# Kernel tuning notes

Measured on AMD Instinct MI355X. Metric: run time of the kernel, lower is better.

Reference implementation:

```python
import jax, jax.numpy as jnp
import numpy as np
import math

B, S, D = 16, 512, 1024
H, L = 16, 4
DH = D // H
EPS = 1e-5


def _layernorm(x, w, b):
    mu = jnp.mean(x, axis=-1, keepdims=True)
    var = jnp.mean(jnp.square(x - mu), axis=-1, keepdims=True)
    return (x - mu) / jnp.sqrt(var + EPS) * w + b


def _pos_encoding(s, d):
    pos = jnp.arange(s, dtype=jnp.float32)[:, None]                      # [s,1]
    div = jnp.exp(jnp.arange(0, d, 2, dtype=jnp.float32) * (-math.log(10000.0) / d))
    ang = pos * div[None, :]                                             # [s,d/2]
    return jnp.stack([jnp.sin(ang), jnp.cos(ang)], axis=-1).reshape(s, d)  # interleave sin/cos


def _attention_layer(x, Wq, bq, Wv, bv, Wo, bo, gamma, ln_w, ln_b, mask):
    bs, s, d = x.shape
    # q_linear == k_linear (kq_same=True)
    q = (x @ Wq.T + bq).reshape(bs, s, H, DH).transpose(0, 2, 1, 3)      # [b,h,s,dh]
    k = q
    v = (x @ Wv.T + bv).reshape(bs, s, H, DH).transpose(0, 2, 1, 3)

    scores = jnp.einsum('bhqd,bhkd->bhqk', q, k) / math.sqrt(DH)         # [b,h,s,s]

    # distance-decay modulation (dist_scores is detached in the original)
    p = jax.nn.softmax(jnp.where(mask, scores, -1e32), axis=-1)
    distcum = jnp.cumsum(p, axis=-1)
    disttot = jnp.sum(p, axis=-1, keepdims=True)
    idx = jnp.arange(s, dtype=jnp.float32)
    pos_eff = jnp.abs(idx[None, :] - idx[:, None])[None, None, :, :]     # |i-j|
    dist = jnp.sqrt(jnp.maximum((disttot - distcum) * pos_eff, 0.0))
    dist = jax.lax.stop_gradient(dist)

    g = -jnp.abs(gamma)[None, :, None, None]                             # [1,h,1,1]
    total_effect = jnp.clip(jnp.exp(dist * g), 1e-5, 1e5)
    scores = scores * total_effect

    scores = jnp.where(mask, scores, -1e32)
    attn = jax.nn.softmax(scores, axis=-1)
    attn = jnp.where(mask, attn, 0.0)

    # maxout=True (peek_cur=False): clamp(1/max, max=5)
    scale = jnp.minimum(1.0 / jnp.max(attn, axis=-1, keepdims=True), 5.0)
    attn = attn * scale

    out = jnp.einsum('bhqk,bhkd->bhqd', attn, v)                         # [b,h,s,dh]
    out = out.transpose(0, 2, 1, 3).reshape(bs, s, d)
    out = out @ Wo.T + bo

    # eval mode: dropout = identity; residual + layernorm
    return _layernorm(x + out, ln_w, ln_b), attn


def reference(x, lens, Wq, bq, Wv, bv, Wo, bo, gammas, ln_w, ln_b, fln_w, fln_b):
    del lens  # only used in training-mode random masking
    s = x.shape[1]
    q = x + _pos_encoding(s, D)[None, :, :]
    mask = jnp.tril(jnp.ones((s, s), dtype=bool), -1)[None, None, :, :]  # peek_cur=False
    scores = None
    for l in range(L):
        q, scores = _attention_layer(q, Wq[l], bq[l], Wv[l], bv[l], Wo[l], bo[l],
                                     gammas[l], ln_w[l], ln_b[l], mask)
    return _layernorm(q, fln_w, fln_b), scores


def setup_inputs() -> dict:
    key = jax.random.key(0)
    ks = jax.random.split(key, 8)
    wscale = 1.0 / math.sqrt(D)
    return {
        'x': jax.random.normal(ks[0], (B, S, D), dtype=jnp.float32),
        'lens': jax.random.randint(ks[1], (B,), 1, S),
        'Wq': jax.random.normal(ks[2], (L, D, D), dtype=jnp.float32) * wscale,
        'bq': jnp.zeros((L, D), dtype=jnp.float32),
        'Wv': jax.random.normal(ks[3], (L, D, D), dtype=jnp.float32) * wscale,
        'bv': jnp.zeros((L, D), dtype=jnp.float32),
        'Wo': jax.random.normal(ks[4], (L, D, D), dtype=jnp.float32) * wscale,
        'bo': jnp.zeros((L, D), dtype=jnp.float32),
        'gammas': jax.random.uniform(ks[5], (L, H), dtype=jnp.float32, minval=-1.7, maxval=1.7),
        'ln_w': jnp.ones((L, D), dtype=jnp.float32),
        'ln_b': jnp.zeros((L, D), dtype=jnp.float32),
        'fln_w': jnp.ones((D,), dtype=jnp.float32),
        'fln_b': jnp.zeros((D,), dtype=jnp.float32),
    }
```

## Files before the change

kernel.cpp:

```cpp
#include <hip/hip_runtime.h>
#include <hip/hip_bf16.h>

#define BB 16
#define SS 512
#define DD 1024
#define HH 16
#define LL 4
#define DHH 64
#define GK 1024

typedef __attribute__((ext_vector_type(8))) short short8;
typedef __attribute__((ext_vector_type(4))) float f32x4;

__device__ __forceinline__ unsigned short f2bf(float f) {
  union { float f; unsigned int u; } v; v.f = f;
  unsigned int r = v.u + 0x7FFFu + ((v.u >> 16) & 1u);
  return (unsigned short)(r >> 16);
}
__device__ __forceinline__ float bf2f(unsigned short u) {
  union { unsigned int i; float f; } v; v.i = ((unsigned)u) << 16; return v.f;
}

__device__ __forceinline__ float wave_max(float v) {
#pragma unroll
  for (int off = 32; off > 0; off >>= 1) v = fmaxf(v, __shfl_xor(v, off));
  return v;
}
__device__ __forceinline__ float wave_sum(float v) {
#pragma unroll
  for (int off = 32; off > 0; off >>= 1) v += __shfl_xor(v, off);
  return v;
}
__device__ __forceinline__ float half_max(float v) {
#pragma unroll
  for (int off = 16; off > 0; off >>= 1) v = fmaxf(v, __shfl_xor(v, off));
  return v;
}
__device__ __forceinline__ float half_sum(float v) {
#pragma unroll
  for (int off = 16; off > 0; off >>= 1) v += __shfl_xor(v, off);
  return v;
}

__device__ __forceinline__ void gl16(const void* g, void* l) {
  __builtin_amdgcn_global_load_lds(
      (const __attribute__((address_space(1))) unsigned int*)(uintptr_t)g,
      (__attribute__((address_space(3))) unsigned int*)(unsigned int)(uintptr_t)l,
      16, 0, 0);
}

__global__ __launch_bounds__(256) void k_w2bf_all(
    const float* __restrict__ wq, const float* __restrict__ wv,
    const float* __restrict__ wo, unsigned short* __restrict__ oqv,
    unsigned short* __restrict__ oo) {
  size_t i4 = ((size_t)blockIdx.x * 256 + threadIdx.x) * 4;
  const size_t QV = (size_t)2 * LL * DD * DD;
  const float* src;
  unsigned short* dst;
  if (i4 < QV) {
    size_t l = i4 >> 21;
    size_t r = i4 & ((1u << 21) - 1);
    src = (r < (1u << 20)) ? wq + (l << 20) + r
                           : wv + (l << 20) + (r - (1u << 20));
    dst = oqv + i4;
  } else {
    size_t j = i4 - QV;
    src = wo + j;
    dst = oo + j;
  }
  float4 v = *(const float4*)src;
  uint2 pk;
  pk.x = (unsigned)f2bf(v.x) | ((unsigned)f2bf(v.y) << 16);
  pk.y = (unsigned)f2bf(v.z) | ((unsigned)f2bf(v.w) << 16);
  *(uint2*)dst = pk;
}

__global__ __launch_bounds__(256) void k_add_pe(const float* __restrict__ x,
                                                unsigned short* __restrict__ outb) {
  size_t i4 = ((size_t)blockIdx.x * 256 + threadIdx.x) * 4;
  int d0 = (int)(i4 & (DD - 1));
  int s = (int)((i4 >> 10) & (SS - 1));
  float4 xv = *(const float4*)(x + i4);
  int ip0 = d0 >> 1;
  float f0 = __expf((float)ip0 * -0.017988946039016f);
  float f1 = __expf((float)(ip0 + 1) * -0.017988946039016f);
  float s0v, c0v, s1v, c1v;
  __sincosf((float)s * f0, &s0v, &c0v);
  __sincosf((float)s * f1, &s1v, &c1v);
  float o0 = xv.x + s0v, o1 = xv.y + c0v, o2 = xv.z + s1v, o3 = xv.w + c1v;
  uint2 pk;
  pk.x = (unsigned)f2bf(o0) | ((unsigned)f2bf(o1) << 16);
  pk.y = (unsigned)f2bf(o2) | ((unsigned)f2bf(o3) << 16);
  *(uint2*)(outb + i4) = pk;
}

template <int MODE>
__global__ __launch_bounds__(256) void k_gemm(
    const unsigned short* __restrict__ A, const unsigned short* __restrict__ W,
    const float* __restrict__ bias, const float* __restrict__ bias2,
    void* __restrict__ out, void* __restrict__ out2) {
  __shared__ unsigned short As[2][128 * 32];
  __shared__ unsigned short Bs[2][128 * 32];
  const int tid = threadIdx.x;
  const int lane = tid & 63;
  const int w = tid >> 6;
  const int wr = w >> 1, wc = w & 1;
  const int fr = lane & 15, fq = lane >> 4;

  int bid = blockIdx.x;
  const int cpx = gridDim.x >> 3;
  bid = (bid & 7) * cpx + (bid >> 3);
  const int bm = (bid & 63) * 128;
  const int bn = (bid >> 6) * 128;

  f32x4 acc[4][4] = {};

  const unsigned short* ga = A + (size_t)(bm + w * 16 + (lane >> 2)) * GK + (lane & 3) * 8;
  const unsigned short* gb = W + (size_t)(bn + w * 16 + (lane >> 2)) * GK + (lane & 3) * 8;

  auto STAGE = [&](int buf, int k0) {
    unsigned short* la = As[buf] + w * 512;
    unsigned short* lb = Bs[buf] + w * 512;
    gl16(ga + k0, la);
    gl16(ga + 64 * GK + k0, la + 2048);
    gl16(gb + k0, lb);
    gl16(gb + 64 * GK + k0, lb + 2048);
  };

  STAGE(0, 0);
  __syncthreads();
  int cur = 0;
  for (int k0 = 0; k0 < GK; k0 += 32) {
    if (k0 + 32 < GK) STAGE(cur ^ 1, k0 + 32);
    short8 af[4], bf[4];
#pragma unroll
    for (int m = 0; m < 4; ++m)
      af[m] = *(const short8*)(As[cur] + (wr * 64 + m * 16 + fr) * 32 + fq * 8);
#pragma unroll
    for (int n = 0; n < 4; ++n)
      bf[n] = *(const short8*)(Bs[cur] + (wc * 64 + n * 16 + fr) * 32 + fq * 8);
#pragma unroll
    for (int m = 0; m < 4; ++m)
#pragma unroll
      for (int n = 0; n < 4; ++n)
        acc[m][n] = __builtin_amdgcn_mfma_f32_16x16x32_bf16(af[m], bf[n], acc[m][n], 0, 0, 0);
    __syncthreads();
    cur ^= 1;
  }

#pragma unroll
  for (int m = 0; m < 4; ++m) {
    const int row0 = bm + wr * 64 + m * 16 + fq * 4;
#pragma unroll
    for (int n = 0; n < 4; ++n) {
      const int col = bn + wc * 64 + n * 16 + fr;
      if constexpr (MODE == 0) {
        const float bsv = bias[col];
        unsigned short* o = (unsigned short*)out;
#pragma unroll
        for (int r = 0; r < 4; ++r)
          o[(size_t)(row0 + r) * DD + col] = f2bf(acc[m][n][r] + bsv);
      } else {
        if (col < DD) {
          const float bsv = bias[col];
          unsigned short* o = (unsigned short*)out;
#pragma unroll
          for (int r = 0; r < 4; ++r)
            o[(size_t)(row0 + r) * DD + col] = f2bf(acc[m][n][r] + bsv);
        } else {
          const int c2 = col - DD;
          const float bsv = bias2[c2];
          unsigned short* o = (unsigned short*)out2;
          const int bi = row0 >> 9, si = row0 & (SS - 1);
          uint2 pk;
          pk.x = (unsigned)f2bf(acc[m][n][0] + bsv) | ((unsigned)f2bf(acc[m][n][1] + bsv) << 16);
          pk.y = (unsigned)f2bf(acc[m][n][2] + bsv) | ((unsigned)f2bf(acc[m][n][3] + bsv) << 16);
          *(uint2*)(o + ((size_t)bi * DD + c2) * SS + si) = pk;
        }
      }
    }
  }
}

__global__ __launch_bounds__(512) void k_attn(
    const unsigned short* __restrict__ Q, const unsigned short* __restrict__ Vt,
    const float* __restrict__ gam, unsigned short* __restrict__ AO,
    float* __restrict__ scores_out) {
  __shared__ float sc_s[32][516];
  __shared__ unsigned short KV[64][72];

  const int tid = threadIdx.x;
  const int lane = tid & 63;
  const int w = tid >> 6;
  const int wr = w & 1;
  const int wc = w >> 1;
  const int fr = lane & 15, fq = lane >> 4;

  const int itile = 15 - (blockIdx.x >> 8);
  const int bh = blockIdx.x & 255;
  const int b = bh >> 4;
  const int h = bh & 15;
  const int i0 = itile * 32;
  const int njt = (itile + 2) >> 1;
  const int jcap = njt * 64;

  const unsigned short* Qb = Q + (size_t)b * SS * DD + h * DHH;
  const unsigned short* Vtb = Vt + ((size_t)b * DD + h * DHH) * SS;
  const float gneg = -fabsf(gam[h]);

  const int srow = tid >> 3;
  const int sdb = (tid & 7) * 8;

  const unsigned short* qrow = Qb + (size_t)(i0 + wr * 16 + fr) * DD;
  short8 a0 = *(const short8*)(qrow + fq * 8);
  short8 a1 = *(const short8*)(qrow + 32 + fq * 8);

  short8 kreg = *(const short8*)(Qb + (size_t)srow * DD + sdb);
  for (int jt = 0; jt < njt; ++jt) {
    *(short8*)&KV[srow][sdb] = kreg;
    const unsigned short* nsrc = (jt + 1 < njt)
        ? Qb + (size_t)((jt + 1) * 64 + srow) * DD + sdb
        : Vtb + (size_t)srow * SS + sdb;
    kreg = *(const short8*)nsrc;
    __syncthreads();

    short8 b0 = *(const short8*)&KV[wc * 16 + fr][fq * 8];
    short8 b1 = *(const short8*)&KV[wc * 16 + fr][32 + fq * 8];
    f32x4 s0 = {};
    __builtin_amdgcn_s_setprio(1);
    s0 = __builtin_amdgcn_mfma_f32_16x16x32_bf16(a0, b0, s0, 0, 0, 0);
    s0 = __builtin_amdgcn_mfma_f32_16x16x32_bf16(a1, b1, s0, 0, 0, 0);
    __builtin_amdgcn_s_setprio(0);

    const int j = jt * 64 + wc * 16 + fr;
#pragma unroll
    for (int r = 0; r < 4; ++r) {
      const int row = wr * 16 + fq * 4 + r;
      sc_s[row][j] = (j < i0 + row) ? s0[r] * 0.125f : -1e30f;
    }
    __syncthreads();
  }
  *(short8*)&KV[srow][sdb] = kreg;

  if (itile >= 8) {
    const int jb = lane << 3;
#pragma unroll 2
    for (int q = 0; q < 4; ++q) {
      const int r_i = w * 4 + q;
      const int gi = i0 + r_i;
      const float* rowp = &sc_s[r_i][0];
      float4 v0 = *(const float4*)(rowp + jb);
      float4 v1 = *(const float4*)(rowp + jb + 4);
      float sc[8] = {v0.x, v0.y, v0.z, v0.w, v1.x, v1.y, v1.z, v1.w};
#pragma unroll
      for (int c = 0; c < 8; ++c)
        if (jb + c >= jcap) sc[c] = -1e30f;

      float p[8];
      float lsum = 0.0f;
#pragma unroll
      for (int c = 0; c < 8; ++c) {
        p[c] = __expf(sc[c]);
        lsum += p[c];
      }

      float xs = lsum;
#pragma unroll
      for (int off = 1; off < 64; off <<= 1) {
        float y = __shfl_up(xs, off);
        if (lane >= off) xs += y;
      }
      const float tot = __shfl(xs, 63);
      const float inv = 1.0f / tot;
      float run = xs - lsum;

      float s2[8];
#pragma unroll
      for (int c = 0; c < 8; ++c) {
        run += p[c];
        float cum = run * inv;
        float dist = sqrtf(fmaxf((1.0f - cum) * (float)(gi - (jb + c)), 0.0f));
        float te = __expf(gneg * dist);
        te = fminf(fmaxf(te, 1e-5f), 1e5f);
        s2[c] = sc[c] * te;
      }

      float m2 = s2[0];
#pragma unroll
      for (int c = 1; c < 8; ++c) m2 = fmaxf(m2, s2[c]);
      m2 = wave_max(m2);
      float e[8];
      float lsum2 = 0.0f;
#pragma unroll
      for (int c = 0; c < 8; ++c) {
        e[c] = __expf(s2[c] - m2);
        lsum2 += e[c];
      }
      float tot2 = wave_sum(lsum2);
      float mult = fminf(tot2, 5.0f) / tot2;

      float av[8];
#pragma unroll
      for (int c = 0; c < 8; ++c) av[c] = (gi == 0) ? 0.0f : e[c] * mult;

      if (scores_out) {
        float* so = scores_out + ((size_t)(b * HH + h) * SS + gi) * SS + jb;
        *(float4*)(so) = make_float4(av[0], av[1], av[2], av[3]);
        *(float4*)(so + 4) = make_float4(av[4], av[5], av[6], av[7]);
      }

      short8 pk;
#pragma unroll
      for (int c = 0; c < 8; ++c) pk[c] = (short)f2bf(av[c]);
      *(short8*)((unsigned short*)&sc_s[r_i][0] + jb) = pk;
    }
  } else {
    const int half = lane >> 5;
    const int ll = lane & 31;
    const int jb = ll << 3;
    for (int q = 0; q < 2; ++q) {
      const int r_i = w * 4 + q * 2 + half;
      const int gi = i0 + r_i;
      const float* rowp = &sc_s[r_i][0];
      float4 v0 = *(const float4*)(rowp + jb);
      float4 v1 = *(const float4*)(rowp + jb + 4);
      float sc[8] = {v0.x, v0.y, v0.z, v0.w, v1.x, v1.y, v1.z, v1.w};
#pragma unroll
      for (int c = 0; c < 8; ++c)
        if (jb + c >= jcap) sc[c] = -1e30f;

      float p[8];
      float lsum = 0.0f;
#pragma unroll
      for (int c = 0; c < 8; ++c) {
        p[c] = __expf(sc[c]);
        lsum += p[c];
      }

      float xs = lsum;
#pragma unroll
      for (int off = 1; off < 32; off <<= 1) {
        float y = __shfl_up(xs, off, 32);
        if (ll >= off) xs += y;
      }
      const float tot = __shfl(xs, 31, 32);
      const float inv = 1.0f / tot;
      float run = xs - lsum;

      float s2[8];
#pragma unroll
      for (int c = 0; c < 8; ++c) {
        run += p[c];
        float cum = run * inv;
        float dist = sqrtf(fmaxf((1.0f - cum) * (float)(gi - (jb + c)), 0.0f));
        float te = __expf(gneg * dist);
        te = fminf(fmaxf(te, 1e-5f), 1e5f);
        s2[c] = sc[c] * te;
      }

      float m2 = s2[0];
#pragma unroll
      for (int c = 1; c < 8; ++c) m2 = fmaxf(m2, s2[c]);
      m2 = half_max(m2);
      float e[8];
      float lsum2 = 0.0f;
#pragma unroll
      for (int c = 0; c < 8; ++c) {
        e[c] = __expf(s2[c] - m2);
        lsum2 += e[c];
      }
      const float tot2 = half_sum(lsum2);
      const float mult = fminf(tot2, 5.0f) / tot2;

      float av[8];
#pragma unroll
      for (int c = 0; c < 8; ++c) av[c] = (gi == 0) ? 0.0f : e[c] * mult;

      if (scores_out) {
        float* so = scores_out + ((size_t)(b * HH + h) * SS + gi) * SS + jb;
        *(float4*)(so) = make_float4(av[0], av[1], av[2], av[3]);
        *(float4*)(so + 4) = make_float4(av[4], av[5], av[6], av[7]);
        *(float4*)(so + 256) = make_float4(0.f, 0.f, 0.f, 0.f);
        *(float4*)(so + 260) = make_float4(0.f, 0.f, 0.f, 0.f);
      }

      short8 pk;
#pragma unroll
      for (int c = 0; c < 8; ++c) pk[c] = (short)f2bf(av[c]);
      *(short8*)((unsigned short*)&sc_s[r_i][0] + jb) = pk;
    }
  }
  __syncthreads();

  short8 vreg;
  if (njt > 1) vreg = *(const short8*)(Vtb + (size_t)srow * SS + 64 + sdb);
  f32x4 o0 = {};
  for (int jt = 0; jt < njt; ++jt) {
    const unsigned short* arow = (const unsigned short*)&sc_s[wr * 16 + fr][0];
    short8 pa0 = *(const short8*)(arow + jt * 64 + fq * 8);
    short8 pa1 = *(const short8*)(arow + jt * 64 + 32 + fq * 8);
    short8 c0 = *(const short8*)&KV[wc * 16 + fr][fq * 8];
    short8 c1 = *(const short8*)&KV[wc * 16 + fr][32 + fq * 8];
    __builtin_amdgcn_s_setprio(1);
    o0 = __builtin_amdgcn_mfma_f32_16x16x32_bf16(pa0, c0, o0, 0, 0, 0);
    o0 = __builtin_amdgcn_mfma_f32_16x16x32_bf16(pa1, c1, o0, 0, 0, 0);
    __builtin_amdgcn_s_setprio(0);
    __syncthreads();
    if (jt + 1 < njt) {
      *(short8*)&KV[srow][sdb] = vreg;
      if (jt + 2 < njt) vreg = *(const short8*)(Vtb + (size_t)srow * SS + (jt + 2) * 64 + sdb);
      __syncthreads();
    }
  }

  {
    const int d = h * DHH + wc * 16 + fr;
#pragma unroll
    for (int r = 0; r < 4; ++r) {
      const int row = i0 + wr * 16 + fq * 4 + r;
      AO[((size_t)b * SS + row) * DD + d] = f2bf(o0[r]);
    }
  }
}

__global__ __launch_bounds__(256) void k_res_ln(
    const unsigned short* __restrict__ x, const unsigned short* __restrict__ r,
    const float* __restrict__ w, const float* __restrict__ b,
    unsigned short* __restrict__ outb, float* __restrict__ outf) {
  __shared__ float red[4];
  const int row = blockIdx.x;
  const int tid = threadIdx.x;
  const int lane = tid & 63, wv = tid >> 6;
  uint2 xa = ((const uint2*)(x + (size_t)row * DD))[tid];
  float y0 = bf2f((unsigned short)xa.x);
  float y1 = bf2f((unsigned short)(xa.x >> 16));
  float y2 = bf2f((unsigned short)xa.y);
  float y3 = bf2f((unsigned short)(xa.y >> 16));
  if (r) {
    uint2 ra = ((const uint2*)(r + (size_t)row * DD))[tid];
    y0 += bf2f((unsigned short)ra.x);
    y1 += bf2f((unsigned short)(ra.x >> 16));
    y2 += bf2f((unsigned short)ra.y);
    y3 += bf2f((unsigned short)(ra.y >> 16));
  }
  float s = y0 + y1 + y2 + y3;
  s = wave_sum(s);
  if (lane == 0) red[wv] = s;
  __syncthreads();
  float mean = (red[0] + red[1] + red[2] + red[3]) * (1.0f / DD);
  __syncthreads();
  float d0 = y0 - mean, d1 = y1 - mean, d2 = y2 - mean, d3 = y3 - mean;
  float s2 = d0 * d0 + d1 * d1 + d2 * d2 + d3 * d3;
  s2 = wave_sum(s2);
  if (lane == 0) red[wv] = s2;
  __syncthreads();
  float var = (red[0] + red[1] + red[2] + red[3]) * (1.0f / DD);
  float rstd = rsqrtf(var + 1e-5f);
  float4 ww = ((const float4*)w)[tid];
  float4 bb = ((const float4*)b)[tid];
  float o0 = d0 * rstd * ww.x + bb.x;
  float o1 = d1 * rstd * ww.y + bb.y;
  float o2 = d2 * rstd * ww.z + bb.z;
  float o3 = d3 * rstd * ww.w + bb.w;
  if (outf) {
    ((float4*)(outf + (size_t)row * DD))[tid] = make_float4(o0, o1, o2, o3);
  } else {
    uint2 pk;
    pk.x = (unsigned)f2bf(o0) | ((unsigned)f2bf(o1) << 16);
    pk.y = (unsigned)f2bf(o2) | ((unsigned)f2bf(o3) << 16);
    ((uint2*)(outb + (size_t)row * DD))[tid] = pk;
  }
}

extern "C" void kernel_launch(void* const* d_in, const int* in_sizes, int n_in,
                              void* d_out, int out_size, void* d_ws, size_t ws_size,
                              hipStream_t stream) {
  (void)in_sizes; (void)n_in; (void)out_size; (void)ws_size;
  const float* x = (const float*)d_in[0];
  const float* Wq = (const float*)d_in[2];
  const float* bq = (const float*)d_in[3];
  const float* Wv = (const float*)d_in[4];
  const float* bv = (const float*)d_in[5];
  const float* Wo = (const float*)d_in[6];
  const float* bo = (const float*)d_in[7];
  const float* gam = (const float*)d_in[8];
  const float* lnw = (const float*)d_in[9];
  const float* lnb = (const float*)d_in[10];
  const float* flnw = (const float*)d_in[11];
  const float* flnb = (const float*)d_in[12];

  float* out0 = (float*)d_out;
  float* scores = out0 + (size_t)BB * SS * DD;
  const size_t BUF = (size_t)BB * SS * DD;
  const size_t WSZ = (size_t)LL * DD * DD;
  const size_t BHSS = (size_t)BB * HH * SS * SS;

  unsigned short* us = (unsigned short*)d_ws;
  unsigned short* Abf0 = us;
  unsigned short* Abf1 = us + BUF;
  unsigned short* Qbf = us + 2 * BUF;
  unsigned short* VtB = us + 3 * BUF;
  unsigned short* AObf = us + 4 * BUF;
  unsigned short* Pb = us + 5 * BUF;
  unsigned short* Wob = us + 6 * BUF;
  unsigned short* Wqvb = (unsigned short*)scores + (2 * BHSS - 2 * WSZ);

  const int M = BB * SS;

  k_w2bf_all<<<dim3(3 * WSZ / 1024), 256, 0, stream>>>(Wq, Wv, Wo, Wqvb, Wob);
  k_add_pe<<<dim3(BUF / 1024), 256, 0, stream>>>(x, Abf0);

  unsigned short* Acur = Abf0;
  unsigned short* Anx = Abf1;
  for (int l = 0; l < LL; ++l) {
    float* sc_dst = (l == LL - 1) ? scores : nullptr;
    k_gemm<3><<<dim3(1024), 256, 0, stream>>>(Acur, Wqvb + (size_t)l * 2048 * DD,
                                              bq + l * DD, bv + l * DD, Qbf, VtB);
    k_attn<<<dim3(BB * HH * 16), 512, 0, stream>>>(Qbf, VtB, gam + l * HH, AObf, sc_dst);
    k_gemm<0><<<dim3(512), 256, 0, stream>>>(AObf, Wob + (size_t)l * DD * DD,
                                             bo + l * DD, nullptr, Pb, nullptr);
    k_res_ln<<<dim3(M), 256, 0, stream>>>(Acur, Pb, lnw + l * DD, lnb + l * DD, Anx, nullptr);
    unsigned short* t = Acur; Acur = Anx; Anx = t;
  }
  k_res_ln<<<dim3(M), 256, 0, stream>>>(Acur, nullptr, flnw, flnb, nullptr, out0);
}
```

Baseline: 820.8 us.

## Double attention query tile to 64 rows and store scores in fp16 LDS

The attention kernel now handles 64 query rows per block instead of 32. Each wave computes two 16-column MFMA tiles, and the grid is halved. Score staging in shared memory moves from fp32 to fp16 so the larger tile fits in about the same LDS footprint. Each K/V tile loaded into LDS is now reused by twice as many query rows, which cuts global reloads and the number of blocks. In exchange, causal tiles get coarser (more wasted work on the diagonal) and intermediate scores lose precision to fp16 before the softmax.

After: 786.7 us. 1.04x faster.

```diff
diff --git a/kernel.cpp b/kernel.cpp
--- a/kernel.cpp
+++ b/kernel.cpp
@@ -11,6 +11,7 @@
 
 typedef __attribute__((ext_vector_type(8))) short short8;
 typedef __attribute__((ext_vector_type(4))) float f32x4;
+typedef __attribute__((ext_vector_type(8))) _Float16 half8;
 
 __device__ __forceinline__ unsigned short f2bf(float f) {
   union { float f; unsigned int u; } v; v.f = f;
@@ -186,22 +187,22 @@
     const unsigned short* __restrict__ Q, const unsigned short* __restrict__ Vt,
     const float* __restrict__ gam, unsigned short* __restrict__ AO,
     float* __restrict__ scores_out) {
-  __shared__ float sc_s[32][516];
+  __shared__ _Float16 sc_s[64][520];
   __shared__ unsigned short KV[64][72];
 
   const int tid = threadIdx.x;
   const int lane = tid & 63;
   const int w = tid >> 6;
-  const int wr = w & 1;
-  const int wc = w >> 1;
+  const int wr = w & 3;
+  const int wc = w >> 2;
   const int fr = lane & 15, fq = lane >> 4;
 
-  const int itile = 15 - (blockIdx.x >> 8);
+  const int itile = 7 - (blockIdx.x >> 8);
   const int bh = blockIdx.x & 255;
   const int b = bh >> 4;
   const int h = bh & 15;
-  const int i0 = itile * 32;
-  const int njt = (itile + 2) >> 1;
+  const int i0 = itile * 64;
+  const int njt = itile + 1;
   const int jcap = njt * 64;
 
   const unsigned short* Qb = Q + (size_t)b * SS * DD + h * DHH;
@@ -224,34 +225,42 @@
     kreg = *(const short8*)nsrc;
     __syncthreads();
 
-    short8 b0 = *(const short8*)&KV[wc * 16 + fr][fq * 8];
-    short8 b1 = *(const short8*)&KV[wc * 16 + fr][32 + fq * 8];
-    f32x4 s0 = {};
+    short8 b00 = *(const short8*)&KV[wc * 32 + fr][fq * 8];
+    short8 b01 = *(const short8*)&KV[wc * 32 + fr][32 + fq * 8];
+    short8 b10 = *(const short8*)&KV[wc * 32 + 16 + fr][fq * 8];
+    short8 b11 = *(const short8*)&KV[wc * 32 + 16 + fr][32 + fq * 8];
+    f32x4 s0 = {}, s1 = {};
     __builtin_amdgcn_s_setprio(1);
-    s0 = __builtin_amdgcn_mfma_f32_16x16x32_bf16(a0, b0, s0, 0, 0, 0);
-    s0 = __builtin_amdgcn_mfma_f32_16x16x32_bf16(a1, b1, s0, 0, 0, 0);
+    s0 = __builtin_amdgcn_mfma_f32_16x16x32_bf16(a0, b00, s0, 0, 0, 0);
+    s0 = __builtin_amdgcn_mfma_f32_16x16x32_bf16(a1, b01, s0, 0, 0, 0);
+    s1 = __builtin_amdgcn_mfma_f32_16x16x32_bf16(a0, b10, s1, 0, 0, 0);
+    s1 = __builtin_amdgcn_mfma_f32_16x16x32_bf16(a1, b11, s1, 0, 0, 0);
     __builtin_amdgcn_s_setprio(0);
 
-    const int j = jt * 64 + wc * 16 + fr;
-#pragma unroll
-    for (int r = 0; r < 4; ++r) {
-      const int row = wr * 16 + fq * 4 + r;
-      sc_s[row][j] = (j < i0 + row) ? s0[r] * 0.125f : -1e30f;
+#pragma unroll
+    for (int n = 0; n < 2; ++n) {
+      const int j = jt * 64 + wc * 32 + n * 16 + fr;
+#pragma unroll
+      for (int r = 0; r < 4; ++r) {
+        const int row = wr * 16 + fq * 4 + r;
+        const float val = (n ? s1[r] : s0[r]) * 0.125f;
+        sc_s[row][j] = (j < i0 + row) ? (_Float16)val : (_Float16)(-65504.0f);
+      }
     }
     __syncthreads();
   }
   *(short8*)&KV[srow][sdb] = kreg;
 
-  if (itile >= 8) {
+  if (itile >= 4) {
     const int jb = lane << 3;
 #pragma unroll 2
-    for (int q = 0; q < 4; ++q) {
-      const int r_i = w * 4 + q;
+    for (int q = 0; q < 8; ++q) {
+      const int r_i = w * 8 + q;
       const int gi = i0 + r_i;
-      const float* rowp = &sc_s[r_i][0];
-      float4 v0 = *(const float4*)(rowp + jb);
-      float4 v1 = *(const float4*)(rowp + jb + 4);
-      float sc[8] = {v0.x, v0.y, v0.z, v0.w, v1.x, v1.y, v1.z, v1.w};
+      half8 hv = *(const half8*)(&sc_s[r_i][0] + jb);
+      float sc[8];
+#pragma unroll
+      for (int c = 0; c < 8; ++c) sc[c] = (float)hv[c];
 #pragma unroll
       for (int c = 0; c < 8; ++c)
         if (jb + c >= jcap) sc[c] = -1e30f;
@@ -318,13 +327,13 @@
     const int half = lane >> 5;
     const int ll = lane & 31;
     const int jb = ll << 3;
-    for (int q = 0; q < 2; ++q) {
-      const int r_i = w * 4 + q * 2 + half;
+    for (int q = 0; q < 4; ++q) {
+      const int r_i = w * 8 + q * 2 + half;
       const int gi = i0 + r_i;
-      const float* rowp = &sc_s[r_i][0];
-      float4 v0 = *(const float4*)(rowp + jb);
-      float4 v1 = *(const float4*)(rowp + jb + 4);
-      float sc[8] = {v0.x, v0.y, v0.z, v0.w, v1.x, v1.y, v1.z, v1.w};
+      half8 hv = *(const half8*)(&sc_s[r_i][0] + jb);
+      float sc[8];
+#pragma unroll
+      for (int c = 0; c < 8; ++c) sc[c] = (float)hv[c];
 #pragma unroll
       for (int c = 0; c < 8; ++c)
         if (jb + c >= jcap) sc[c] = -1e30f;
@@ -394,16 +403,20 @@
 
   short8 vreg;
   if (njt > 1) vreg = *(const short8*)(Vtb + (size_t)srow * SS + 64 + sdb);
-  f32x4 o0 = {};
+  f32x4 o0 = {}, o1 = {};
   for (int jt = 0; jt < njt; ++jt) {
     const unsigned short* arow = (const unsigned short*)&sc_s[wr * 16 + fr][0];
     short8 pa0 = *(const short8*)(arow + jt * 64 + fq * 8);
     short8 pa1 = *(const short8*)(arow + jt * 64 + 32 + fq * 8);
-    short8 c0 = *(const short8*)&KV[wc * 16 + fr][fq * 8];
-    short8 c1 = *(const short8*)&KV[wc * 16 + fr][32 + fq * 8];
+    short8 c00 = *(const short8*)&KV[wc * 32 + fr][fq * 8];
+    short8 c01 = *(const short8*)&KV[wc * 32 + fr][32 + fq * 8];
+    short8 c10 = *(const short8*)&KV[wc * 32 + 16 + fr][fq * 8];
+    short8 c11 = *(const short8*)&KV[wc * 32 + 16 + fr][32 + fq * 8];
     __builtin_amdgcn_s_setprio(1);
-    o0 = __builtin_amdgcn_mfma_f32_16x16x32_bf16(pa0, c0, o0, 0, 0, 0);
-    o0 = __builtin_amdgcn_mfma_f32_16x16x32_bf16(pa1, c1, o0, 0, 0, 0);
+    o0 = __builtin_amdgcn_mfma_f32_16x16x32_bf16(pa0, c00, o0, 0, 0, 0);
+    o0 = __builtin_amdgcn_mfma_f32_16x16x32_bf16(pa1, c01, o0, 0, 0, 0);
+    o1 = __builtin_amdgcn_mfma_f32_16x16x32_bf16(pa0, c10, o1, 0, 0, 0);
+    o1 = __builtin_amdgcn_mfma_f32_16x16x32_bf16(pa1, c11, o1, 0, 0, 0);
     __builtin_amdgcn_s_setprio(0);
     __syncthreads();
     if (jt + 1 < njt) {
@@ -413,12 +426,13 @@
     }
   }
 
-  {
-    const int d = h * DHH + wc * 16 + fr;
+#pragma unroll
+  for (int n = 0; n < 2; ++n) {
+    const int d = h * DHH + wc * 32 + n * 16 + fr;
 #pragma unroll
     for (int r = 0; r < 4; ++r) {
       const int row = i0 + wr * 16 + fq * 4 + r;
-      AO[((size_t)b * SS + row) * DD + d] = f2bf(o0[r]);
+      AO[((size_t)b * SS + row) * DD + d] = f2bf(n ? o1[r] : o0[r]);
     }
   }
 }
@@ -516,7 +530,7 @@
     float* sc_dst = (l == LL - 1) ? scores : nullptr;
     k_gemm<3><<<dim3(1024), 256, 0, stream>>>(Acur, Wqvb + (size_t)l * 2048 * DD,
                                               bq + l * DD, bv + l * DD, Qbf, VtB);
-    k_attn<<<dim3(BB * HH * 16), 512, 0, stream>>>(Qbf, VtB, gam + l * HH, AObf, sc_dst);
+    k_attn<<<dim3(BB * HH * 8), 512, 0, stream>>>(Qbf, VtB, gam + l * HH, AObf, sc_dst);
     k_gemm<0><<<dim3(512), 256, 0, stream>>>(AObf, Wob + (size_t)l * DD * DD,
                                              bo + l * DD, nullptr, Pb, nullptr);
     k_res_ln<<<dim3(M), 256, 0, stream>>>(Acur, Pb, lnw + l * DD, lnb + l * DD, Anx, nullptr);
```
